# Kernel optimization log

Measured on AMD Instinct MI355X. Metric: run time of the kernel, lower is better.

Reference implementation:

```python
import jax, jax.numpy as jnp
import numpy as np

D_MODEL = 1024
NUM_HEADS = 16
D_K = D_MODEL // NUM_HEADS
BATCH = 4
SEQ = 2048


def setup_inputs() -> dict:
    key = jax.random.key(0)
    ks = jax.random.split(key, 12)
    s = 0.02
    inp = {
        "Q": jax.random.normal(ks[0], (BATCH, SEQ, D_MODEL), jnp.float32),
        "K": jax.random.normal(ks[1], (BATCH, SEQ, D_MODEL), jnp.float32),
        "V": jax.random.normal(ks[2], (BATCH, SEQ, D_MODEL), jnp.float32),
        "mask": jnp.tril(jnp.ones((SEQ, SEQ), jnp.int32)),  # causal: 0 = masked
        "Wq": jax.random.normal(ks[3], (D_MODEL, D_MODEL), jnp.float32) * s,
        "bq": jax.random.normal(ks[4], (D_MODEL,), jnp.float32) * s,
        "Wk": jax.random.normal(ks[5], (D_MODEL, D_MODEL), jnp.float32) * s,
        "bk": jax.random.normal(ks[6], (D_MODEL,), jnp.float32) * s,
        "Wv": jax.random.normal(ks[7], (D_MODEL, D_MODEL), jnp.float32) * s,
        "bv": jax.random.normal(ks[8], (D_MODEL,), jnp.float32) * s,
        "Wo": jax.random.normal(ks[9], (D_MODEL, D_MODEL), jnp.float32) * s,
        "bo": jax.random.normal(ks[10], (D_MODEL,), jnp.float32) * s,
    }
    return inp


def _split_heads(x):
    # (b, s, d_model) -> (b, h, s, d_k)
    b, s, _ = x.shape
    return x.reshape(b, s, NUM_HEADS, D_K).transpose(0, 2, 1, 3)


def reference(Q, K, V, mask, Wq, bq, Wk, bk, Wv, bv, Wo, bo):
    # Linear projections (torch Linear: x @ W^T + b)
    q = _split_heads(Q @ Wq.T + bq)  # (b, h, s, dk)
    k = _split_heads(K @ Wk.T + bk)
    v = _split_heads(V @ Wv.T + bv)
    scale = 1.0 / jnp.sqrt(jnp.asarray(D_K, q.dtype))
    scores = jnp.einsum("bhqd,bhkd->bhqk", q, k) * scale  # (b, h, s, s)
    scores = jnp.where(mask == 0, jnp.asarray(-jnp.inf, scores.dtype), scores)
    attn = jax.nn.softmax(scores, axis=-1)
    out = jnp.einsum("bhqk,bhkd->bhqd", attn, v)  # (b, h, s, dk)
    b, h, s, dk = out.shape
    out = out.transpose(0, 2, 1, 3).reshape(b, s, h * dk)  # combine heads
    return out @ Wo.T + bo
```

## Files before the change

kernel.cpp:

```cpp
#include <hip/hip_runtime.h>


typedef _Float16 f16;
typedef _Float16 f16x8 __attribute__((ext_vector_type(8)));
typedef _Float16 f16x4 __attribute__((ext_vector_type(4)));
typedef float floatx4 __attribute__((ext_vector_type(4)));

#define SEQ 2048
#define DM 1024
#define NH 16
#define DK 64
#define MR 8192

#define QSCALE 0.18033688011112042f

#if __has_builtin(__builtin_amdgcn_exp2f)
#define EXP2(x) __builtin_amdgcn_exp2f(x)
#else
#define EXP2(x) __expf(0.6931471805599453f * (x))
#endif

__device__ __forceinline__ void gl_lds16(const void* g, void* lds) {
    __builtin_amdgcn_global_load_lds(
        (const __attribute__((address_space(1))) unsigned int*)g,
        (__attribute__((address_space(3))) unsigned int*)lds,
        16, 0, 0);
}

struct ConvArgs {
    const float* s[7];
    f16* d[7];
};

__global__ __launch_bounds__(256) void convk(ConvArgs a) {
    int bx = blockIdx.x;
    int t, base;
    if (bx < 3 * 8192) { t = bx / 8192; base = bx - t * 8192; }
    else { int r = bx - 3 * 8192; t = 3 + r / 1024; base = r - (t - 3) * 1024; }
    int i = base * 256 + threadIdx.x;
    float4 v = ((const float4*)a.s[t])[i];
    f16x4 o;
    o.x = (f16)v.x; o.y = (f16)v.y; o.z = (f16)v.z; o.w = (f16)v.w;
    ((f16x4*)a.d[t])[i] = o;
}

template <int MODE>
__device__ __forceinline__ void gemm_body(
    const f16* __restrict__ A, const f16* __restrict__ W,
    const float* __restrict__ bias, void* __restrict__ outp,
    int m0, int n0, float oscale, f16* As, f16* Bs)
{
    const int tid = threadIdx.x;
    const int wave = tid >> 6, lane = tid & 63;
    const int quad = lane >> 4, ln = lane & 15;
    const int wr = wave >> 1, wc = wave & 1;

    floatx4 acc[4][4] = {};

    for (int kt = 0; kt < 16; ++kt) {
        const int k0 = kt * 64;
#pragma unroll
        for (int s = 0; s < 4; ++s) {
            int c = s * 256 + tid;
            int row = c >> 3, lc = (c & 7) ^ (row & 7);
            gl_lds16(A + (size_t)(m0 + row) * 1024 + k0 + lc * 8,
                     (char*)As + (s * 256 + wave * 64) * 16);
        }
#pragma unroll
        for (int s = 0; s < 4; ++s) {
            int c = s * 256 + tid;
            int row = c >> 3, lc = (c & 7) ^ (row & 7);
            gl_lds16(W + (size_t)(n0 + row) * 1024 + k0 + lc * 8,
                     (char*)Bs + (s * 256 + wave * 64) * 16);
        }
        __syncthreads();
#pragma unroll
        for (int kk = 0; kk < 64; kk += 32) {
            const int cb = kk >> 3;
            f16x8 af[4], bf[4];
#pragma unroll
            for (int i = 0; i < 4; ++i) {
                int row = wr * 64 + i * 16 + ln;
                af[i] = *(const f16x8*)&As[row * 64 + (((cb + quad) ^ (ln & 7)) << 3)];
            }
#pragma unroll
            for (int j = 0; j < 4; ++j) {
                int row = wc * 64 + j * 16 + ln;
                bf[j] = *(const f16x8*)&Bs[row * 64 + (((cb + quad) ^ (ln & 7)) << 3)];
            }
#pragma unroll
            for (int i = 0; i < 4; ++i)
#pragma unroll
                for (int j = 0; j < 4; ++j)
                    acc[i][j] = __builtin_amdgcn_mfma_f32_16x16x32_f16(
                        af[i], bf[j], acc[i][j], 0, 0, 0);
        }
        __syncthreads();
    }

#pragma unroll
    for (int i = 0; i < 4; ++i) {
#pragma unroll
        for (int j = 0; j < 4; ++j) {
            int col = n0 + wc * 64 + j * 16 + ln;
            float bc = bias[col];
            int rowb = m0 + wr * 64 + i * 16 + quad * 4;
#pragma unroll
            for (int r = 0; r < 4; ++r) {
                float v = (acc[i][j][r] + bc) * oscale;
                int rm = rowb + r;
                if (MODE == 2) {
                    ((float*)outp)[(size_t)rm * 1024 + col] = v;
                } else {
                    int bb = rm >> 11, ss = rm & 2047;
                    int hh = col >> 6, dd = col & 63;
                    f16* o = (f16*)outp;
                    if (MODE == 0)
                        o[(((size_t)(bb * 16 + hh)) * 2048 + ss) * 64 + dd] = (f16)v;
                    else
                        o[(((size_t)(bb * 16 + hh)) * 64 + dd) * 2048 + ss] = (f16)v;
                }
            }
        }
    }
}

struct G3Args {
    const f16* A[3]; const f16* W[3]; const float* b[3]; f16* o[3];
};

__global__ __launch_bounds__(256, 2) void gemm_qkv(G3Args g) {
    __shared__ alignas(16) f16 As[128 * 64];
    __shared__ alignas(16) f16 Bs[128 * 64];
    const int z = blockIdx.z;
    const int m0 = blockIdx.x * 128, n0 = blockIdx.y * 128;
    if (z < 2)
        gemm_body<0>(g.A[z], g.W[z], g.b[z], g.o[z], m0, n0,
                     z == 0 ? QSCALE : 1.0f, As, Bs);
    else
        gemm_body<1>(g.A[2], g.W[2], g.b[2], g.o[2], m0, n0, 1.0f, As, Bs);
}

__global__ __launch_bounds__(256, 2) void gemm_out(
    const f16* __restrict__ A, const f16* __restrict__ W,
    const float* __restrict__ bias, float* __restrict__ outp)
{
    __shared__ alignas(16) f16 As[128 * 64];
    __shared__ alignas(16) f16 Bs[128 * 64];
    gemm_body<2>(A, W, bias, outp, blockIdx.x * 128, blockIdx.y * 128, 1.0f, As, Bs);
}

__global__ __launch_bounds__(256, 2) void attn_kernel(
    const f16* __restrict__ Qp, const f16* __restrict__ Kp,
    const f16* __restrict__ Vt, f16* __restrict__ Op)
{
    __shared__ alignas(16) f16 ks[128 * 64];
    __shared__ alignas(16) f16 vs[64 * 128];
    __shared__ alignas(16) f16 ps[128 * 128];

    const int tid = threadIdx.x;
    const int wave = tid >> 6, lane = tid & 63;
    const int quad = lane >> 4, ln = lane & 15;
    const int bh = blockIdx.x;
    const f16* qb = Qp + (size_t)bh * SEQ * DK;
    const f16* kb = Kp + (size_t)bh * SEQ * DK;
    const f16* vb = Vt + (size_t)bh * DK * SEQ;
    const int b = bh >> 4, h = bh & 15;

    f16* pslot = ps + wave * 4096;

    f16x8 ones;
#pragma unroll
    for (int e = 0; e < 8; ++e) ones[e] = (f16)1.0f;

    for (int half = 0; half < 2; ++half) {
        const int jt = half ? (15 - blockIdx.y) : blockIdx.y;
        const int q0 = jt * 128;

#pragma unroll
        for (int s = 0; s < 4; ++s) {
            int c = s * 256 + tid;
            int row = c >> 3, lc = (c & 7) ^ (row & 7);
            gl_lds16(qb + (size_t)(q0 + row) * 64 + lc * 8,
                     (char*)ps + (s * 256 + wave * 64) * 16);
        }
        __syncthreads();
        f16x8 aq[2][2];
#pragma unroll
        for (int mt = 0; mt < 2; ++mt)
#pragma unroll
            for (int kk = 0; kk < 2; ++kk) {
                int row = wave * 32 + mt * 16 + ln;
                aq[mt][kk] = *(const f16x8*)&ps[row * 64 + (((kk * 4 + quad) ^ (ln & 7)) << 3)];
            }

        floatx4 oacc[2][4] = {};
        floatx4 lacc[2] = {};

        const int nk = jt + 1;
        for (int kt = 0; kt < nk; ++kt) {
            const int k0 = kt * 128;
#pragma unroll
            for (int s = 0; s < 4; ++s) {
                int c = s * 256 + tid;
                int row = c >> 3, lc = (c & 7) ^ (row & 7);
                gl_lds16(kb + (size_t)(k0 + row) * 64 + lc * 8,
                         (char*)ks + (s * 256 + wave * 64) * 16);
            }
#pragma unroll
            for (int s = 0; s < 4; ++s) {
                int c = s * 256 + tid;
                int row = c >> 4, lc = (c & 15) ^ (row & 15);
                gl_lds16(vb + (size_t)row * SEQ + k0 + lc * 8,
                         (char*)vs + (s * 256 + wave * 64) * 16);
            }
            __syncthreads();

            floatx4 sacc[2][8] = {};
#pragma unroll
            for (int kk = 0; kk < 2; ++kk) {
                const int pc = ((kk * 4 + quad) ^ (ln & 7)) << 3;
#pragma unroll
                for (int nt = 0; nt < 8; ++nt) {
                    f16x8 bk = *(const f16x8*)&ks[(nt * 16 + ln) * 64 + pc];
#pragma unroll
                    for (int mt = 0; mt < 2; ++mt)
                        sacc[mt][nt] = __builtin_amdgcn_mfma_f32_16x16x32_f16(
                            bk, aq[mt][kk], sacc[mt][nt], 0, 0, 0);
                }
            }

            const bool diag = (k0 == q0);
#pragma unroll
            for (int mt = 0; mt < 2; ++mt) {
                const int rp = mt * 16 + ln;
                const int qrow = q0 + wave * 32 + rp;
                f16* prow = pslot + rp * 128;
#pragma unroll
                for (int nt = 0; nt < 8; ++nt) {
                    const int kbase = k0 + nt * 16 + quad * 4;
                    f16x4 pk;
#pragma unroll
                    for (int r = 0; r < 4; ++r) {
                        float t = sacc[mt][nt][r];
                        if (diag && kbase + r > qrow) t = -1e30f;
                        pk[r] = (f16)EXP2(t);
                    }
                    const int ch = nt * 2 + (quad >> 1);
                    *(f16x4*)&prow[((ch ^ ln) << 3) + (quad & 1) * 4] = pk;
                }
            }

#pragma unroll
            for (int kk4 = 0; kk4 < 4; ++kk4) {
                f16x8 ap[2];
#pragma unroll
                for (int mt = 0; mt < 2; ++mt) {
                    int rp = mt * 16 + ln;
                    ap[mt] = *(const f16x8*)&pslot[rp * 128 + (((kk4 * 4 + quad) ^ ln) << 3)];
                    lacc[mt] = __builtin_amdgcn_mfma_f32_16x16x32_f16(
                        ap[mt], ones, lacc[mt], 0, 0, 0);
                }
#pragma unroll
                for (int nt2 = 0; nt2 < 4; ++nt2) {
                    int row = nt2 * 16 + ln;
                    f16x8 bv = *(const f16x8*)&vs[row * 128 + (((kk4 * 4 + quad) ^ ln) << 3)];
#pragma unroll
                    for (int mt = 0; mt < 2; ++mt)
                        oacc[mt][nt2] = __builtin_amdgcn_mfma_f32_16x16x32_f16(
                            ap[mt], bv, oacc[mt][nt2], 0, 0, 0);
                }
            }
            __syncthreads();
        }

#pragma unroll
        for (int mt = 0; mt < 2; ++mt) {
            int rowb = q0 + wave * 32 + mt * 16 + quad * 4;
            float inv[4];
#pragma unroll
            for (int r = 0; r < 4; ++r) inv[r] = 1.0f / lacc[mt][r];
#pragma unroll
            for (int nt2 = 0; nt2 < 4; ++nt2) {
                int col = h * 64 + nt2 * 16 + ln;
#pragma unroll
                for (int r = 0; r < 4; ++r) {
                    float v = oacc[mt][nt2][r] * inv[r];
                    Op[((size_t)b * SEQ + rowb + r) * DM + col] = (f16)v;
                }
            }
        }
    }
}

extern "C" void kernel_launch(void* const* d_in, const int* in_sizes, int n_in,
                              void* d_out, int out_size, void* d_ws, size_t ws_size,
                              hipStream_t stream) {
    const float* Q  = (const float*)d_in[0];
    const float* K  = (const float*)d_in[1];
    const float* V  = (const float*)d_in[2];
    const float* Wq = (const float*)d_in[4];
    const float* bq = (const float*)d_in[5];
    const float* Wk = (const float*)d_in[6];
    const float* bk = (const float*)d_in[7];
    const float* Wv = (const float*)d_in[8];
    const float* bv = (const float*)d_in[9];
    const float* Wo = (const float*)d_in[10];
    const float* bo = (const float*)d_in[11];

    char* ws = (char*)d_ws;
    f16* Xq  = (f16*)(ws);
    f16* Xk  = Xq + (size_t)MR * DM;
    f16* Xv  = Xk + (size_t)MR * DM;
    f16* Wqb = Xv + (size_t)MR * DM;
    f16* Wkb = Wqb + (size_t)DM * DM;
    f16* Wvb = Wkb + (size_t)DM * DM;
    f16* Wob = Wvb + (size_t)DM * DM;
    f16* qp  = Wob + (size_t)DM * DM;
    f16* kp  = qp + (size_t)MR * DM;
    f16* vtp = kp + (size_t)MR * DM;

    ConvArgs ca;
    ca.s[0] = Q;  ca.d[0] = Xq;
    ca.s[1] = K;  ca.d[1] = Xk;
    ca.s[2] = V;  ca.d[2] = Xv;
    ca.s[3] = Wq; ca.d[3] = Wqb;
    ca.s[4] = Wk; ca.d[4] = Wkb;
    ca.s[5] = Wv; ca.d[5] = Wvb;
    ca.s[6] = Wo; ca.d[6] = Wob;
    convk<<<3 * 8192 + 4 * 1024, 256, 0, stream>>>(ca);

    G3Args g;
    g.A[0] = Xq; g.W[0] = Wqb; g.b[0] = bq; g.o[0] = qp;
    g.A[1] = Xk; g.W[1] = Wkb; g.b[1] = bk; g.o[1] = kp;
    g.A[2] = Xv; g.W[2] = Wvb; g.b[2] = bv; g.o[2] = vtp;
    gemm_qkv<<<dim3(64, 8, 3), 256, 0, stream>>>(g);

    attn_kernel<<<dim3(64, 8), 256, 0, stream>>>(qp, kp, vtp, Xq);

    gemm_out<<<dim3(64, 8), 256, 0, stream>>>(Xq, Wob, bo, (float*)d_out);
}
```

Before: 319.1 us.

## Keep attention probabilities in registers via 32x32 MFMA and permlane swap

Rewrites the attention inner loop to use 32x32x16 MFMAs so the exp'd score tile can be repacked in registers with v_permlane32_swap and fed directly as the A operand of the PV matmul. This removes the 32KB per-block LDS buffer for P and its write/read round trip, and the Q staging reuses the K buffer instead. The smaller LDS footprint allows raising launch bounds to 3 blocks per CU. Costs include an extra sync after Q load, and the register pressure implied by targeting 3 blocks per CU.

```diff
diff --git a/kernel.cpp b/kernel.cpp
--- a/kernel.cpp
+++ b/kernel.cpp
@@ -5,6 +5,8 @@
 typedef _Float16 f16x8 __attribute__((ext_vector_type(8)));
 typedef _Float16 f16x4 __attribute__((ext_vector_type(4)));
 typedef float floatx4 __attribute__((ext_vector_type(4)));
+typedef float f32x16 __attribute__((ext_vector_type(16)));
+typedef unsigned int uint4v __attribute__((ext_vector_type(4)));
 
 #define SEQ 2048
 #define DM 1024
@@ -150,24 +152,21 @@
     gemm_body<2>(A, W, bias, outp, blockIdx.x * 128, blockIdx.y * 128, 1.0f, As, Bs);
 }
 
-__global__ __launch_bounds__(256, 2) void attn_kernel(
+__global__ __launch_bounds__(256, 3) void attn_kernel(
     const f16* __restrict__ Qp, const f16* __restrict__ Kp,
     const f16* __restrict__ Vt, f16* __restrict__ Op)
 {
     __shared__ alignas(16) f16 ks[128 * 64];
     __shared__ alignas(16) f16 vs[64 * 128];
-    __shared__ alignas(16) f16 ps[128 * 128];
 
     const int tid = threadIdx.x;
     const int wave = tid >> 6, lane = tid & 63;
-    const int quad = lane >> 4, ln = lane & 15;
+    const int h = lane >> 5, c31 = lane & 31;
     const int bh = blockIdx.x;
     const f16* qb = Qp + (size_t)bh * SEQ * DK;
-    const f16* kb = Kp + (size_t)bh * SEQ * DK;
+    const f16* kbp = Kp + (size_t)bh * SEQ * DK;
     const f16* vb = Vt + (size_t)bh * DK * SEQ;
-    const int b = bh >> 4, h = bh & 15;
-
-    f16* pslot = ps + wave * 4096;
+    const int b = bh >> 4, hd = bh & 15;
 
     f16x8 ones;
 #pragma unroll
@@ -182,20 +181,18 @@
             int c = s * 256 + tid;
             int row = c >> 3, lc = (c & 7) ^ (row & 7);
             gl_lds16(qb + (size_t)(q0 + row) * 64 + lc * 8,
-                     (char*)ps + (s * 256 + wave * 64) * 16);
+                     (char*)ks + (s * 256 + wave * 64) * 16);
         }
         __syncthreads();
-        f16x8 aq[2][2];
-#pragma unroll
-        for (int mt = 0; mt < 2; ++mt)
-#pragma unroll
-            for (int kk = 0; kk < 2; ++kk) {
-                int row = wave * 32 + mt * 16 + ln;
-                aq[mt][kk] = *(const f16x8*)&ps[row * 64 + (((kk * 4 + quad) ^ (ln & 7)) << 3)];
-            }
-
-        floatx4 oacc[2][4] = {};
-        floatx4 lacc[2] = {};
+        f16x8 bq[4];
+#pragma unroll
+        for (int t = 0; t < 4; ++t) {
+            int row = wave * 32 + c31;
+            bq[t] = *(const f16x8*)&ks[row * 64 + (((2 * t + h) ^ (row & 7)) << 3)];
+        }
+        __syncthreads();
+
+        f32x16 oacc0 = {}, oacc1 = {}, lacc = {};
 
         const int nk = jt + 1;
         for (int kt = 0; kt < nk; ++kt) {
@@ -204,7 +201,7 @@
             for (int s = 0; s < 4; ++s) {
                 int c = s * 256 + tid;
                 int row = c >> 3, lc = (c & 7) ^ (row & 7);
-                gl_lds16(kb + (size_t)(k0 + row) * 64 + lc * 8,
+                gl_lds16(kbp + (size_t)(k0 + row) * 64 + lc * 8,
                          (char*)ks + (s * 256 + wave * 64) * 16);
             }
 #pragma unroll
@@ -216,78 +213,77 @@
             }
             __syncthreads();
 
-            floatx4 sacc[2][8] = {};
-#pragma unroll
-            for (int kk = 0; kk < 2; ++kk) {
-                const int pc = ((kk * 4 + quad) ^ (ln & 7)) << 3;
-#pragma unroll
-                for (int nt = 0; nt < 8; ++nt) {
-                    f16x8 bk = *(const f16x8*)&ks[(nt * 16 + ln) * 64 + pc];
-#pragma unroll
-                    for (int mt = 0; mt < 2; ++mt)
-                        sacc[mt][nt] = __builtin_amdgcn_mfma_f32_16x16x32_f16(
-                            bk, aq[mt][kk], sacc[mt][nt], 0, 0, 0);
+            const bool diag = (kt == jt);
+            const int qloc = wave * 32 + c31;
+
+#pragma unroll
+            for (int kb = 0; kb < 4; ++kb) {
+                f32x16 sacc = {};
+#pragma unroll
+                for (int t = 0; t < 4; ++t) {
+                    int row = kb * 32 + c31;
+                    f16x8 ak = *(const f16x8*)&ks[row * 64 + (((2 * t + h) ^ (row & 7)) << 3)];
+                    sacc = __builtin_amdgcn_mfma_f32_32x32x16_f16(
+                        ak, bq[t], sacc, 0, 0, 0);
                 }
-            }
-
-            const bool diag = (k0 == q0);
-#pragma unroll
-            for (int mt = 0; mt < 2; ++mt) {
-                const int rp = mt * 16 + ln;
-                const int qrow = q0 + wave * 32 + rp;
-                f16* prow = pslot + rp * 128;
-#pragma unroll
-                for (int nt = 0; nt < 8; ++nt) {
-                    const int kbase = k0 + nt * 16 + quad * 4;
-                    f16x4 pk;
-#pragma unroll
-                    for (int r = 0; r < 4; ++r) {
-                        float t = sacc[mt][nt][r];
-                        if (diag && kbase + r > qrow) t = -1e30f;
-                        pk[r] = (f16)EXP2(t);
+
+                unsigned pg[4][2];
+#pragma unroll
+                for (int g = 0; g < 4; ++g) {
+#pragma unroll
+                    for (int j = 0; j < 2; ++j) {
+                        const int r = 4 * g + 2 * j;
+                        const int kg = kb * 32 + 8 * g + 4 * h + 2 * j;
+                        float s0 = sacc[r], s1 = sacc[r + 1];
+                        float p0 = (diag && kg > qloc) ? 0.0f : EXP2(s0);
+                        float p1 = (diag && kg + 1 > qloc) ? 0.0f : EXP2(s1);
+                        auto pp = __builtin_amdgcn_cvt_pkrtz(p0, p1);
+                        pg[g][j] = __builtin_bit_cast(unsigned, pp);
                     }
-                    const int ch = nt * 2 + (quad >> 1);
-                    *(f16x4*)&prow[((ch ^ ln) << 3) + (quad & 1) * 4] = pk;
                 }
-            }
-
-#pragma unroll
-            for (int kk4 = 0; kk4 < 4; ++kk4) {
-                f16x8 ap[2];
-#pragma unroll
-                for (int mt = 0; mt < 2; ++mt) {
-                    int rp = mt * 16 + ln;
-                    ap[mt] = *(const f16x8*)&pslot[rp * 128 + (((kk4 * 4 + quad) ^ ln) << 3)];
-                    lacc[mt] = __builtin_amdgcn_mfma_f32_16x16x32_f16(
-                        ap[mt], ones, lacc[mt], 0, 0, 0);
+
+#pragma unroll
+                for (int sub = 0; sub < 2; ++sub) {
+                    const int s = 2 * kb + sub;
+                    unsigned a0 = pg[2 * sub][0], a1 = pg[2 * sub][1];
+                    unsigned b0 = pg[2 * sub + 1][0], b1 = pg[2 * sub + 1][1];
+                    asm("v_permlane32_swap_b32 %0, %1" : "+v"(a0), "+v"(b0));
+                    asm("v_permlane32_swap_b32 %0, %1" : "+v"(a1), "+v"(b1));
+                    uint4v fw;
+                    fw.x = a0; fw.y = a1; fw.z = b0; fw.w = b1;
+                    f16x8 F = __builtin_bit_cast(f16x8, fw);
+
+                    lacc = __builtin_amdgcn_mfma_f32_32x32x16_f16(
+                        F, ones, lacc, 0, 0, 0);
+                    {
+                        int row = c31;
+                        f16x8 bv = *(const f16x8*)&vs[row * 128 + (((2 * s + h) ^ (row & 15)) << 3)];
+                        oacc0 = __builtin_amdgcn_mfma_f32_32x32x16_f16(
+                            F, bv, oacc0, 0, 0, 0);
+                    }
+                    {
+                        int row = 32 + c31;
+                        f16x8 bv = *(const f16x8*)&vs[row * 128 + (((2 * s + h) ^ (row & 15)) << 3)];
+                        oacc1 = __builtin_amdgcn_mfma_f32_32x32x16_f16(
+                            F, bv, oacc1, 0, 0, 0);
+                    }
                 }
-#pragma unroll
-                for (int nt2 = 0; nt2 < 4; ++nt2) {
-                    int row = nt2 * 16 + ln;
-                    f16x8 bv = *(const f16x8*)&vs[row * 128 + (((kk4 * 4 + quad) ^ ln) << 3)];
-#pragma unroll
-                    for (int mt = 0; mt < 2; ++mt)
-                        oacc[mt][nt2] = __builtin_amdgcn_mfma_f32_16x16x32_f16(
-                            ap[mt], bv, oacc[mt][nt2], 0, 0, 0);
-                }
             }
             __syncthreads();
         }
 
 #pragma unroll
-        for (int mt = 0; mt < 2; ++mt) {
-            int rowb = q0 + wave * 32 + mt * 16 + quad * 4;
-            float inv[4];
-#pragma unroll
-            for (int r = 0; r < 4; ++r) inv[r] = 1.0f / lacc[mt][r];
-#pragma unroll
-            for (int nt2 = 0; nt2 < 4; ++nt2) {
-                int col = h * 64 + nt2 * 16 + ln;
-#pragma unroll
-                for (int r = 0; r < 4; ++r) {
-                    float v = oacc[mt][nt2][r] * inv[r];
-                    Op[((size_t)b * SEQ + rowb + r) * DM + col] = (f16)v;
-                }
+        for (int r = 0; r < 16; ++r) {
+            const int qr = (r & 3) + 8 * (r >> 2) + 4 * h;
+            const int rowg = q0 + wave * 32 + qr;
+            float inv = 1.0f / lacc[r];
+            {
+                int col = hd * 64 + c31;
+                Op[((size_t)b * SEQ + rowg) * DM + col] = (f16)(oacc0[r] * inv);
+            }
+            {
+                int col = hd * 64 + 32 + c31;
+                Op[((size_t)b * SEQ + rowg) * DM + col] = (f16)(oacc1[r] * inv);
             }
         }
     }
```

Result: faster. 305.2 us (median of 3 runs) (-4.4%).
